# Kernel optimization log

Hardware: AMD Instinct MI355X
Metric: run time of the kernel (lower is better)

## Reference

```python
import jax, jax.numpy as jnp
import numpy as np

NUM_FEATURES = 129  # lstm_hidden + 1
GAMMA = 1.0


def _lstm(x, W_ih, W_hh, b_ih, b_hh):
    # x: [B,S,F]; W_ih: [4H,F]; W_hh: [4H,H]; gates in torch order i,f,g,o
    B, S, _ = x.shape
    H = W_hh.shape[1]
    xg = jnp.einsum('bsf,gf->bsg', x, W_ih) + b_ih  # [B,S,4H]

    def step(carry, xt):
        h, c = carry
        g = xt + h @ W_hh.T + b_hh
        i, f, gg, o = jnp.split(g, 4, axis=-1)
        c = jax.nn.sigmoid(f) * c + jax.nn.sigmoid(i) * jnp.tanh(gg)
        h = jax.nn.sigmoid(o) * jnp.tanh(c)
        return (h, c), h

    h0 = jnp.zeros((B, H), x.dtype)
    (_, _), hs = jax.lax.scan(step, (h0, h0), jnp.swapaxes(xg, 0, 1))
    return jnp.swapaxes(hs, 0, 1)  # [B,S,H]


def setup_inputs() -> dict:
    key = jax.random.key(0)
    ks = jax.random.split(key, 10)
    B, S, F, H = 16, 2048, 129, 128
    s = 0.05  # keep activations in a sane range
    return {
        'x': jax.random.normal(ks[0], (B, S, F), jnp.float32),
        'prototypes': jax.random.normal(ks[1], (B, S, F), jnp.float32),
        'W_ih': jax.random.normal(ks[2], (4 * H, F), jnp.float32) * s,
        'W_hh': jax.random.normal(ks[3], (4 * H, H), jnp.float32) * s,
        'b_ih': jax.random.normal(ks[4], (4 * H,), jnp.float32) * s,
        'b_hh': jax.random.normal(ks[5], (4 * H,), jnp.float32) * s,
        'Wc': jax.random.normal(ks[6], (4, F, F), jnp.float32) * s,
        'bc': jax.random.normal(ks[7], (4, F), jnp.float32) * s,
        'Wh': jax.random.normal(ks[8], (2, F), jnp.float32) * s,
        'bh': jax.random.normal(ks[9], (2,), jnp.float32) * s,
    }


def reference(x, prototypes, W_ih, W_hh, b_ih, b_hh, Wc, bc, Wh, bh):
    lstm_out = _lstm(x, W_ih, W_hh, b_ih, b_hh)  # [B,S,H]
    # attention path is detached in the original (numpy round-trip)
    q = jax.lax.stop_gradient(lstm_out)
    # note: scale uses num_features (embed_dim of the attention object), not H
    scores = jnp.einsum('bqh,bkh->bqk', q, q) / jnp.sqrt(jnp.float32(NUM_FEATURES))
    attn = jax.nn.softmax(scores, axis=-1)
    context = jnp.einsum('bqk,bkh->bqh', attn, q)  # [B,S,H]
    # vectorized RBF kernel vs prototypes (original does a Python loop per (i,j))
    diff = x - prototypes
    kernel_features = jnp.exp(-GAMMA * jnp.sum(diff * diff, axis=-1, keepdims=True))  # [B,S,1]
    h = jnp.concatenate([context, kernel_features], axis=-1)  # [B,S,NUM_FEATURES]
    for l in range(4):
        h = jax.nn.relu(h @ Wc[l].T + bc[l])
    logits = h @ Wh.T + bh  # [B,S,2]
    return jax.nn.log_softmax(logits, axis=-1)
```

## Files before the change

kernel.cpp:

```cpp
#include <hip/hip_runtime.h>
#include <stdint.h>

#define B_ 16
#define S_ 2048
#define F_ 129
#define H_ 128
#define G_ 512

typedef float f32x4 __attribute__((ext_vector_type(4)));
typedef float f32x4a4 __attribute__((ext_vector_type(4), aligned(4)));
typedef short s16x8 __attribute__((ext_vector_type(8)));
typedef _Float16 f16x8 __attribute__((ext_vector_type(8)));
typedef _Float16 f16x4 __attribute__((ext_vector_type(4)));

#define BAR_LDS() __asm__ volatile("s_waitcnt lgkmcnt(0)\n\ts_barrier" ::: "memory")

#define L2E 1.44269504088896f

__device__ inline unsigned short h2bits(_Float16 h) {
  union { _Float16 h; unsigned short u; } v; v.h = h; return v.u;
}
__device__ inline unsigned short f2h(float f) { return h2bits((_Float16)f); }
__device__ inline float rcp_(float x) { return __builtin_amdgcn_rcpf(x); }
__device__ inline float exp2_(float x) {
  float r; __asm__("v_exp_f32 %0, %1" : "=v"(r) : "v"(x)); return r;
}

__global__ __launch_bounds__(512, 2) void front_kernel(
    const float* __restrict__ x, const float* __restrict__ prot,
    const float* __restrict__ W_ih, const float* __restrict__ W_hh,
    const float* __restrict__ b_ih, const float* __restrict__ b_hh,
    _Float16* __restrict__ xg, unsigned short* __restrict__ qbf,
    float* __restrict__ kf, int* __restrict__ prog) {
  __shared__ __align__(16) char smem[82048];
  int tid = threadIdx.x;
  int blk = blockIdx.x;

  if (blk < 4) {
    _Float16 (*hbuf)[4 * 144] = (_Float16 (*)[4 * 144])smem;
    int w = tid >> 6, lane = tid & 63;
    int n16 = lane & 15;
    int q8 = lane >> 4;
    int ab = n16 >> 2;
    int u = (w << 4) | n16;
    int bb = blk * 4;
    f16x8 Wf[4][4];
    #pragma unroll
    for (int ty = 0; ty < 4; ++ty) {
      float gs = (ty == 2) ? (2.f * L2E) : (-L2E);
      #pragma unroll
      for (int kb = 0; kb < 4; ++kb) {
        const float* src = &W_hh[(ty * 128 + u) * H_ + kb * 32 + q8 * 8];
        f16x8 v;
        #pragma unroll
        for (int j = 0; j < 8; ++j) v[j] = (_Float16)(src[j] * gs);
        Wf[ty][kb] = v;
      }
    }
    for (int i = tid; i < 2 * 4 * 144; i += 512)
      ((_Float16*)hbuf)[i] = (_Float16)0.f;
    float c = 0.f;
    int hoff = ab * 144 + q8 * 8;
    const _Float16* h0 = &hbuf[0][hoff];
    const _Float16* h1 = &hbuf[1][hoff];
    _Float16* hw = &hbuf[0][q8 * 144 + u];
    const int hstride = 4 * 144;
    const _Float16* xb = xg + (long)(bb + q8) * S_ * G_ + u * 4;
    unsigned short* qp = qbf + (long)(bb + q8) * S_ * H_ + u - H_;
    const _Float16* xpf = xb + 4 * G_;
    while (__hip_atomic_load(&prog[0], __ATOMIC_ACQUIRE, __HIP_MEMORY_SCOPE_AGENT) < 16)
      __builtin_amdgcn_s_sleep(2);
    while (__hip_atomic_load(&prog[1], __ATOMIC_ACQUIRE, __HIP_MEMORY_SCOPE_AGENT) < 16)
      __builtin_amdgcn_s_sleep(2);
    f16x4 cur[4];
    #pragma unroll
    for (int p = 0; p < 4; ++p) cur[p] = *(const f16x4*)(xb + (long)p * G_);
    unsigned short hvp = 0;
    __syncthreads();
    for (int t = 0; t < S_; t += 4) {
      if ((t & 63) == 0 && t != 0 && t < 1984) {
        int cn = (t >> 6) + 1;
        while (__hip_atomic_load(&prog[cn], __ATOMIC_ACQUIRE, __HIP_MEMORY_SCOPE_AGENT) < 16)
          __builtin_amdgcn_s_sleep(2);
      }
      #pragma unroll
      for (int p = 0; p < 4; ++p) {
        BAR_LDS();
        const _Float16* hsrc = (p & 1) ? h0 : h1;
        f16x8 A[4];
        #pragma unroll
        for (int kb = 0; kb < 4; ++kb)
          A[kb] = *(const f16x8*)(hsrc + kb * 32);
        if (t + p > 0)
          *qp = hvp;
        qp += H_;
        f16x4 xcur = cur[p];
        cur[p] = *(const f16x4*)xpf;
        xpf += G_;
        f32x4 r0a[4], r1a[4];
        #pragma unroll
        for (int ty = 0; ty < 4; ++ty) {
          f32x4 a0, a1;
          a0[0] = (float)xcur[ty]; a0[1] = 0.f; a0[2] = 0.f; a0[3] = 0.f;
          a1[0] = 0.f; a1[1] = 0.f; a1[2] = 0.f; a1[3] = 0.f;
          a0 = __builtin_amdgcn_mfma_f32_16x16x32_f16(A[0], Wf[ty][0], a0, 0, 0, 0);
          a1 = __builtin_amdgcn_mfma_f32_16x16x32_f16(A[2], Wf[ty][2], a1, 0, 0, 0);
          a0 = __builtin_amdgcn_mfma_f32_16x16x32_f16(A[1], Wf[ty][1], a0, 0, 0, 0);
          a1 = __builtin_amdgcn_mfma_f32_16x16x32_f16(A[3], Wf[ty][3], a1, 0, 0, 0);
          r0a[ty] = a0; r1a[ty] = a1;
        }
        float g0 = r0a[0][0] + r1a[0][0];
        float g1 = r0a[1][0] + r1a[1][0];
        float g2 = r0a[2][0] + r1a[2][0];
        float g3 = r0a[3][0] + r1a[3][0];
        float ai = rcp_(1.f + exp2_(g0));
        float af = rcp_(1.f + exp2_(g1));
        float ag = 1.f - 2.f * rcp_(1.f + exp2_(g2));
        float ao = rcp_(1.f + exp2_(g3));
        c = af * c + ai * ag;
        float th = 1.f - 2.f * rcp_(1.f + exp2_(c * (2.f * L2E)));
        float hv = ao * th;
        _Float16 hf = (_Float16)hv;
        hw[(p & 1) * hstride] = hf;
        hvp = h2bits(hf);
      }
    }
    *qp = hvp;

  } else if (blk < 516) {
    _Float16 (*xs)[136] = (_Float16 (*)[136])smem;
    _Float16 (*ws)[136] = (_Float16 (*)[136])(smem + 17408);
    float* bsum = (float*)(smem + 17408 + 34816);
    int xblk = blk - 4;
    int batch = xblk & 15, chunk = xblk >> 4;
    long R0 = (long)batch * S_ + chunk * 64;
    int lane = tid & 63, w = tid >> 6;
    int tw = w & 3, hi = w >> 2;
    int l15 = lane & 15, q = lane >> 4;
    for (int it = 0; it < 4; ++it) {
      int i = tid + it * 512;
      int r = i >> 5, cx = (i & 31) * 4;
      f32x4a4 v = *(const f32x4a4*)&x[(R0 + r) * 129 + cx];
      f16x4 hq;
      #pragma unroll
      for (int j = 0; j < 4; ++j) hq[j] = (_Float16)v[j];
      *(f16x4*)&xs[r][cx] = hq;
    }
    if (tid < 64) xs[tid][128] = (_Float16)x[(R0 + tid) * 129 + 128];
    bsum[tid] = b_ih[tid] + b_hh[tid];
    __syncthreads();
    f16x8 Bf[4];
    #pragma unroll
    for (int kb = 0; kb < 4; ++kb)
      Bf[kb] = *(const f16x8*)&xs[16 * tw + l15][kb * 32 + q * 8];
    float x128 = (float)xs[16 * tw + l15][128];
    f16x4 res[16];
    #pragma unroll
    for (int cg = 0; cg < 4; ++cg) {
      __syncthreads();
      for (int it = 0; it < 8; ++it) {
        int i = tid + it * 512;
        int r = i >> 5, cc = (i & 31) * 4;
        f32x4a4 v = *(const f32x4a4*)&W_ih[(long)(cg * 128 + r) * 129 + cc];
        f16x4 hq;
        #pragma unroll
        for (int j = 0; j < 4; ++j) hq[j] = (_Float16)v[j];
        *(f16x4*)&ws[r][cc] = hq;
      }
      if (tid < 128) ws[tid][128] = (_Float16)W_ih[(long)(cg * 128 + tid) * 129 + 128];
      __syncthreads();
      float gs = (cg == 2) ? (2.f * L2E) : (-L2E);
      #pragma unroll
      for (int t = 0; t < 4; ++t) {
        int tt = hi * 4 + t;
        f32x4 acc;
        acc[0] = 0.f; acc[1] = 0.f; acc[2] = 0.f; acc[3] = 0.f;
        #pragma unroll
        for (int kb = 0; kb < 4; ++kb) {
          f16x8 Af = *(const f16x8*)&ws[tt * 16 + l15][kb * 32 + q * 8];
          acc = __builtin_amdgcn_mfma_f32_16x16x32_f16(Af, Bf[kb], acc, 0, 0, 0);
        }
        #pragma unroll
        for (int r = 0; r < 4; ++r) {
          int unit = tt * 16 + q * 4 + r;
          float vv = (acc[r] + bsum[cg * 128 + unit] + x128 * (float)ws[unit][128]) * gs;
          res[t * 4 + r][cg] = (_Float16)vv;
        }
      }
    }
    long rowbase = (R0 + 16 * tw + l15) * G_;
    #pragma unroll
    for (int t = 0; t < 4; ++t)
      #pragma unroll
      for (int r = 0; r < 4; ++r)
        *(f16x4*)&xg[rowbase + ((hi * 4 + t) * 16 + q * 4 + r) * 4] = res[t * 4 + r];
    __syncthreads();
    if (tid == 0) {
      __threadfence();
      __hip_atomic_fetch_add(&prog[chunk], 1, __ATOMIC_RELEASE, __HIP_MEMORY_SCOPE_AGENT);
    }

  } else {
    int rblk = blk - 516;
    int wave = tid >> 6, lane = tid & 63;
    for (int it = 0; it < 8; ++it) {
      long row = (long)rblk * 64 + it * 8 + wave;
      const float* xr = x + row * F_;
      const float* pr = prot + row * F_;
      float ss = 0.f;
      for (int k = lane; k < F_; k += 64) { float d = xr[k] - pr[k]; ss += d * d; }
      #pragma unroll
      for (int off = 32; off; off >>= 1) ss += __shfl_xor(ss, off, 64);
      if (lane == 0) kf[row] = __expf(-ss);
    }
  }
}

__global__ __launch_bounds__(256) void back_kernel(
    const unsigned short* __restrict__ qbf, const float* __restrict__ kf,
    const float* __restrict__ Wc, const float* __restrict__ bc,
    const float* __restrict__ Wh, const float* __restrict__ bh,
    float* __restrict__ out) {
  __shared__ __align__(16) char smem[74560];
  _Float16 (*hb)[64][136] = (_Float16 (*)[64][136])smem;
  unsigned short* Ps = (unsigned short*)(smem + 17408);
  unsigned short* Ks = (unsigned short*)(smem + 34816);
  unsigned short* VT = (unsigned short*)(smem + 34816 + 17408);
  _Float16 (*wl)[136] = (_Float16 (*)[136])(smem + 34816);
  float* bl = (float*)(smem + 34816 + 39168);

  int tid = threadIdx.x;
  int lane = tid & 63, w = tid >> 6;
  int b = blockIdx.x >> 5;
  int q0 = (blockIdx.x & 31) * 64;
  long R0 = (long)blockIdx.x * 64;
  const unsigned short* qb = qbf + (long)b * S_ * H_;
  int l15 = lane & 15;
  int q = lane >> 4;
  int koff = q * 8;

  f16x8 qfrag[4];
  #pragma unroll
  for (int kb = 0; kb < 4; ++kb)
    qfrag[kb] = *(const f16x8*)(qb + (long)(q0 + w * 16 + l15) * H_ + kb * 32 + koff);
  f32x4 oacc[8];
  #pragma unroll
  for (int n = 0; n < 8; ++n)
    #pragma unroll
    for (int r = 0; r < 4; ++r) oacc[n][r] = 0.f;
  float mrow[4], lrow[4];
  #pragma unroll
  for (int r = 0; r < 4; ++r) { mrow[r] = -1e30f; lrow[r] = 0.f; }
  const float scale = 0.08804509063256238f;
  unsigned short* Pw = Ps + w * 16 * 72;
  for (int t = 0; t < S_ / 64; ++t) {
    {
      int rr = tid >> 4;
      int c0 = (tid & 15) * 8;
      #pragma unroll
      for (int pch = 0; pch < 4; ++pch) {
        int r = pch * 16 + rr;
        s16x8 v = *(const s16x8*)(qb + (long)(t * 64 + r) * H_ + c0);
        *(s16x8*)(&Ks[r * 136 + c0]) = v;
        int rbase = r >> 3, rl = r & 7;
        #pragma unroll
        for (int i = 0; i < 8; ++i) {
          int d = c0 + i;
          VT[d * 72 + ((rbase ^ ((d >> 3) & 7)) << 3) + rl] = (unsigned short)v[i];
        }
      }
    }
    __syncthreads();
    f32x4 sacc[4];
    #pragma unroll
    for (int n = 0; n < 4; ++n) {
      f32x4 acc;
      #pragma unroll
      for (int r = 0; r < 4; ++r) acc[r] = 0.f;
      #pragma unroll
      for (int kb = 0; kb < 4; ++kb) {
        f16x8 bfrag = *(const f16x8*)(&Ks[(n * 16 + l15) * 136 + kb * 32 + koff]);
        acc = __builtin_amdgcn_mfma_f32_16x16x32_f16(qfrag[kb], bfrag, acc, 0, 0, 0);
      }
      sacc[n] = acc;
    }
    #pragma unroll
    for (int r = 0; r < 4; ++r) {
      float mx = fmaxf(fmaxf(sacc[0][r], sacc[1][r]), fmaxf(sacc[2][r], sacc[3][r]));
      #pragma unroll
      for (int m = 1; m < 16; m <<= 1) mx = fmaxf(mx, __shfl_xor(mx, m, 64));
      mx *= scale;
      float mnew = fmaxf(mrow[r], mx);
      float alpha = __expf(mrow[r] - mnew);
      mrow[r] = mnew;
      float psum = 0.f;
      #pragma unroll
      for (int n = 0; n < 4; ++n) {
        float pv = __expf(sacc[n][r] * scale - mnew);
        sacc[n][r] = pv;
        psum += pv;
      }
      #pragma unroll
      for (int m = 1; m < 16; m <<= 1) psum += __shfl_xor(psum, m, 64);
      lrow[r] = lrow[r] * alpha + psum;
      #pragma unroll
      for (int n = 0; n < 8; ++n) oacc[n][r] *= alpha;
    }
    #pragma unroll
    for (int n = 0; n < 4; ++n)
      #pragma unroll
      for (int r = 0; r < 4; ++r)
        Pw[(q * 4 + r) * 72 + n * 16 + l15] = f2h(sacc[n][r]);
    __syncthreads();
    #pragma unroll
    for (int kb = 0; kb < 2; ++kb) {
      f16x8 afrag = *(const f16x8*)(&Pw[l15 * 72 + kb * 32 + koff]);
      #pragma unroll
      for (int n = 0; n < 8; ++n) {
        int d = n * 16 + l15;
        int rb = ((kb * 32 + koff) >> 3) ^ ((d >> 3) & 7);
        f16x8 bfrag = *(const f16x8*)(&VT[d * 72 + (rb << 3)]);
        oacc[n] = __builtin_amdgcn_mfma_f32_16x16x32_f16(afrag, bfrag, oacc[n], 0, 0, 0);
      }
    }
    __syncthreads();
  }
  float rl4[4];
  #pragma unroll
  for (int r = 0; r < 4; ++r) rl4[r] = rcp_(lrow[r]);
  #pragma unroll
  for (int n = 0; n < 8; ++n)
    #pragma unroll
    for (int r = 0; r < 4; ++r)
      hb[0][w * 16 + q * 4 + r][n * 16 + l15] = (_Float16)(oacc[n][r] * rl4[r]);
  if (tid < 64) hb[0][tid][128] = (_Float16)kf[R0 + tid];

  int cur = 0;
  for (int l = 0; l < 4; ++l) {
    __syncthreads();
    for (int it = 0; it < 18; ++it) {
      int i = tid + it * 256;
      int r = i >> 5, cc = (i & 31) * 4;
      int rs = (r < 129) ? r : 128;
      f32x4a4 v = *(const f32x4a4*)&Wc[((long)l * 129 + rs) * 129 + cc];
      f16x4 hq;
      #pragma unroll
      for (int j = 0; j < 4; ++j) hq[j] = (_Float16)v[j];
      *(f16x4*)&wl[r][cc] = hq;
    }
    if (tid < 144) {
      int rs = (tid < 129) ? tid : 128;
      wl[tid][128] = (_Float16)Wc[((long)l * 129 + rs) * 129 + 128];
      bl[tid] = bc[l * 129 + rs];
    }
    __syncthreads();
    f16x8 Bf[4];
    #pragma unroll
    for (int kb = 0; kb < 4; ++kb)
      Bf[kb] = *(const f16x8*)&hb[cur][16 * w + l15][kb * 32 + q * 8];
    float h128 = (float)hb[cur][16 * w + l15][128];
    int nxt = cur ^ 1;
    #pragma unroll
    for (int t = 0; t < 9; ++t) {
      f32x4 acc;
      acc[0] = 0.f; acc[1] = 0.f; acc[2] = 0.f; acc[3] = 0.f;
      #pragma unroll
      for (int kb = 0; kb < 4; ++kb) {
        f16x8 Af = *(const f16x8*)&wl[t * 16 + l15][kb * 32 + q * 8];
        acc = __builtin_amdgcn_mfma_f32_16x16x32_f16(Af, Bf[kb], acc, 0, 0, 0);
      }
      f16x4 hv;
      #pragma unroll
      for (int r = 0; r < 4; ++r) {
        int u = t * 16 + q * 4 + r;
        float v = acc[r] + bl[u] + h128 * (float)wl[u][128];
        hv[r] = (_Float16)fmaxf(v, 0.f);
      }
      if (t < 8)
        *(f16x4*)&hb[nxt][16 * w + l15][t * 16 + q * 4] = hv;
      else if (q == 0)
        hb[nxt][16 * w + l15][128] = hv[0];
    }
    cur ^= 1;
  }
  __syncthreads();
  if (tid < 128) {
    int row = tid >> 1, j = tid & 1;
    float z = bh[j];
    const float* whp = Wh + j * 129;
    for (int k = 0; k < 129; ++k) z += (float)hb[cur][row][k] * whp[k];
    float zo = __shfl_xor(z, 1, 64);
    float mx = fmaxf(z, zo);
    float lse = mx + __logf(__expf(z - mx) + __expf(zo - mx));
    out[(R0 + row) * 2 + j] = z - lse;
  }
}

extern "C" void kernel_launch(void* const* d_in, const int* in_sizes, int n_in,
                              void* d_out, int out_size, void* d_ws, size_t ws_size,
                              hipStream_t stream) {
  const float* x    = (const float*)d_in[0];
  const float* prot = (const float*)d_in[1];
  const float* W_ih = (const float*)d_in[2];
  const float* W_hh = (const float*)d_in[3];
  const float* b_ih = (const float*)d_in[4];
  const float* b_hh = (const float*)d_in[5];
  const float* Wc   = (const float*)d_in[6];
  const float* bc   = (const float*)d_in[7];
  const float* Wh   = (const float*)d_in[8];
  const float* bh   = (const float*)d_in[9];
  float* out = (float*)d_out;
  char* ws = (char*)d_ws;
  _Float16* xgh       = (_Float16*)(ws);
  unsigned short* qbf = (unsigned short*)(ws + 33554432);
  float* kf           = (float*)(ws + 41943040);
  int* prog           = (int*)(ws + 42074112);

  hipMemsetAsync(prog, 0, 128, stream);
  hipLaunchKernelGGL(front_kernel, dim3(1028), dim3(512), 0, stream,
                     x, prot, W_ih, W_hh, b_ih, b_hh, xgh, qbf, kf, prog);
  hipLaunchKernelGGL(back_kernel, dim3(512), dim3(256), 0, stream,
                     qbf, kf, Wc, bc, Wh, bh, out);
}
```

Baseline: 1.131 ms.

## Write transposed LSTM output from recurrence and load V tile directly; single-thread flag polling

The recurrent blocks now also write each hidden value into a transposed [B,H,S] buffer, so the attention kernel can load the V^T tile with vectorized 16-byte reads instead of scattering eight scalar LDS stores per element. Spin-waiting on progress flags now happens on one thread with a longer sleep and a deadline, followed by a block barrier, rather than every thread polling. The cost is an extra strided scalar global store per step in the serial LSTM loop, plus more barriers in that loop. The deadline escape could also let the loop continue before its producers finish if they are slow.

```diff
diff --git a/kernel.cpp b/kernel.cpp
--- a/kernel.cpp
+++ b/kernel.cpp
@@ -26,15 +26,30 @@
   float r; __asm__("v_exp_f32 %0, %1" : "=v"(r) : "v"(x)); return r;
 }
 
+__device__ inline void wait_flag(int* f, int tgt, int tid, long deadline) {
+  if (tid == 0) {
+    if (__hip_atomic_load(f, __ATOMIC_RELAXED, __HIP_MEMORY_SCOPE_AGENT) < tgt) {
+      while (__hip_atomic_load(f, __ATOMIC_RELAXED, __HIP_MEMORY_SCOPE_AGENT) < tgt) {
+        __builtin_amdgcn_s_sleep(32);
+        if ((long)__builtin_amdgcn_s_memrealtime() > deadline) break;
+      }
+    }
+    (void)__hip_atomic_load(f, __ATOMIC_ACQUIRE, __HIP_MEMORY_SCOPE_AGENT);
+  }
+  __syncthreads();
+}
+
 __global__ __launch_bounds__(512, 2) void front_kernel(
     const float* __restrict__ x, const float* __restrict__ prot,
     const float* __restrict__ W_ih, const float* __restrict__ W_hh,
     const float* __restrict__ b_ih, const float* __restrict__ b_hh,
     _Float16* __restrict__ xg, unsigned short* __restrict__ qbf,
-    float* __restrict__ kf, int* __restrict__ prog) {
+    unsigned short* __restrict__ qbfT, float* __restrict__ kf,
+    int* __restrict__ prog) {
   __shared__ __align__(16) char smem[82048];
   int tid = threadIdx.x;
   int blk = blockIdx.x;
+  long deadline = (long)__builtin_amdgcn_s_memrealtime() + 4000000L;
 
   if (blk < 4) {
     _Float16 (*hbuf)[4 * 144] = (_Float16 (*)[4 * 144])smem;
@@ -67,22 +82,18 @@
     const int hstride = 4 * 144;
     const _Float16* xb = xg + (long)(bb + q8) * S_ * G_ + u * 4;
     unsigned short* qp = qbf + (long)(bb + q8) * S_ * H_ + u - H_;
+    unsigned short* qpT = qbfT + ((long)(bb + q8) * H_ + u) * S_ - 1;
     const _Float16* xpf = xb + 4 * G_;
-    while (__hip_atomic_load(&prog[0], __ATOMIC_ACQUIRE, __HIP_MEMORY_SCOPE_AGENT) < 16)
-      __builtin_amdgcn_s_sleep(2);
-    while (__hip_atomic_load(&prog[1], __ATOMIC_ACQUIRE, __HIP_MEMORY_SCOPE_AGENT) < 16)
-      __builtin_amdgcn_s_sleep(2);
+    wait_flag(&prog[0], 16, tid, deadline);
+    wait_flag(&prog[1], 16, tid, deadline);
     f16x4 cur[4];
     #pragma unroll
     for (int p = 0; p < 4; ++p) cur[p] = *(const f16x4*)(xb + (long)p * G_);
     unsigned short hvp = 0;
     __syncthreads();
     for (int t = 0; t < S_; t += 4) {
-      if ((t & 63) == 0 && t != 0 && t < 1984) {
-        int cn = (t >> 6) + 1;
-        while (__hip_atomic_load(&prog[cn], __ATOMIC_ACQUIRE, __HIP_MEMORY_SCOPE_AGENT) < 16)
-          __builtin_amdgcn_s_sleep(2);
-      }
+      if ((t & 63) == 0 && t != 0 && t < 1984)
+        wait_flag(&prog[(t >> 6) + 1], 16, tid, deadline);
       #pragma unroll
       for (int p = 0; p < 4; ++p) {
         BAR_LDS();
@@ -91,9 +102,12 @@
         #pragma unroll
         for (int kb = 0; kb < 4; ++kb)
           A[kb] = *(const f16x8*)(hsrc + kb * 32);
-        if (t + p > 0)
+        if (t + p > 0) {
           *qp = hvp;
+          *qpT = hvp;
+        }
         qp += H_;
+        qpT += 1;
         f16x4 xcur = cur[p];
         cur[p] = *(const f16x4*)xpf;
         xpf += G_;
@@ -126,6 +140,7 @@
       }
     }
     *qp = hvp;
+    *qpT = hvp;
 
   } else if (blk < 516) {
     _Float16 (*xs)[136] = (_Float16 (*)[136])smem;
@@ -217,7 +232,8 @@
 }
 
 __global__ __launch_bounds__(256) void back_kernel(
-    const unsigned short* __restrict__ qbf, const float* __restrict__ kf,
+    const unsigned short* __restrict__ qbf, const unsigned short* __restrict__ qbfT,
+    const float* __restrict__ kf,
     const float* __restrict__ Wc, const float* __restrict__ bc,
     const float* __restrict__ Wh, const float* __restrict__ bh,
     float* __restrict__ out) {
@@ -235,6 +251,7 @@
   int q0 = (blockIdx.x & 31) * 64;
   long R0 = (long)blockIdx.x * 64;
   const unsigned short* qb = qbf + (long)b * S_ * H_;
+  const unsigned short* qbT = qbfT + (long)b * H_ * S_;
   int l15 = lane & 15;
   int q = lane >> 4;
   int koff = q * 8;
@@ -260,14 +277,15 @@
       #pragma unroll
       for (int pch = 0; pch < 4; ++pch) {
         int r = pch * 16 + rr;
-        s16x8 v = *(const s16x8*)(qb + (long)(t * 64 + r) * H_ + c0);
-        *(s16x8*)(&Ks[r * 136 + c0]) = v;
-        int rbase = r >> 3, rl = r & 7;
-        #pragma unroll
-        for (int i = 0; i < 8; ++i) {
-          int d = c0 + i;
-          VT[d * 72 + ((rbase ^ ((d >> 3) & 7)) << 3) + rl] = (unsigned short)v[i];
-        }
+        *(s16x8*)(&Ks[r * 136 + c0]) =
+            *(const s16x8*)(qb + (long)(t * 64 + r) * H_ + c0);
+      }
+      #pragma unroll
+      for (int vt = 0; vt < 4; ++vt) {
+        int idx = tid + vt * 256;
+        int d = idx >> 3, tg = idx & 7;
+        s16x8 v = *(const s16x8*)(qbT + (long)d * S_ + t * 64 + tg * 8);
+        *(s16x8*)(&VT[d * 72 + ((tg ^ ((d >> 3) & 7)) << 3)]) = v;
       }
     }
     __syncthreads();
@@ -411,14 +429,15 @@
   const float* bh   = (const float*)d_in[9];
   float* out = (float*)d_out;
   char* ws = (char*)d_ws;
-  _Float16* xgh       = (_Float16*)(ws);
-  unsigned short* qbf = (unsigned short*)(ws + 33554432);
-  float* kf           = (float*)(ws + 41943040);
-  int* prog           = (int*)(ws + 42074112);
+  _Float16* xgh        = (_Float16*)(ws);
+  unsigned short* qbf  = (unsigned short*)(ws + 33554432);
+  unsigned short* qbfT = (unsigned short*)(ws + 41943040);
+  float* kf            = (float*)(ws + 50331648);
+  int* prog            = (int*)(ws + 50462720);
 
   hipMemsetAsync(prog, 0, 128, stream);
   hipLaunchKernelGGL(front_kernel, dim3(1028), dim3(512), 0, stream,
-                     x, prot, W_ih, W_hh, b_ih, b_hh, xgh, qbf, kf, prog);
+                     x, prot, W_ih, W_hh, b_ih, b_hh, xgh, qbf, qbfT, kf, prog);
   hipLaunchKernelGGL(back_kernel, dim3(512), dim3(256), 0, stream,
-                     qbf, kf, Wc, bc, Wh, bh, out);
-}
+                     qbf, qbfT, kf, Wc, bc, Wh, bh, out);
+}
```

New measurement: 1.334 ms. 1.18x slower.

## Prefetch next K/V tile into registers, raise MFMA priority, single-thread flag waits

Applied to the files above, without the earlier changes.

The attention loop now loads the next 64-row K/V tile from global memory into registers while the current tile is written into LDS, so global load latency overlaps with compute. MFMA sections are wrapped in s_setprio to favour matrix work across waves. The LSTM blocks' spin-waits on producer progress flags are changed so one thread polls with a longer sleep and a timeout, then the block synchronises, which cuts polling traffic from every thread. The timeout could let the LSTM read data before it is ready if producers are slow, and the prefetch adds register pressure.

```diff
diff --git a/kernel.cpp b/kernel.cpp
--- a/kernel.cpp
+++ b/kernel.cpp
@@ -24,6 +24,19 @@
 __device__ inline float rcp_(float x) { return __builtin_amdgcn_rcpf(x); }
 __device__ inline float exp2_(float x) {
   float r; __asm__("v_exp_f32 %0, %1" : "=v"(r) : "v"(x)); return r;
+}
+
+__device__ inline void wait_flag(int* f, int tgt, int tid, long deadline) {
+  if (tid == 0) {
+    if (__hip_atomic_load(f, __ATOMIC_RELAXED, __HIP_MEMORY_SCOPE_AGENT) < tgt) {
+      while (__hip_atomic_load(f, __ATOMIC_RELAXED, __HIP_MEMORY_SCOPE_AGENT) < tgt) {
+        __builtin_amdgcn_s_sleep(32);
+        if ((long)__builtin_amdgcn_s_memrealtime() > deadline) break;
+      }
+    }
+    (void)__hip_atomic_load(f, __ATOMIC_ACQUIRE, __HIP_MEMORY_SCOPE_AGENT);
+  }
+  __syncthreads();
 }
 
 __global__ __launch_bounds__(512, 2) void front_kernel(
@@ -35,6 +48,7 @@
   __shared__ __align__(16) char smem[82048];
   int tid = threadIdx.x;
   int blk = blockIdx.x;
+  long deadline = (long)__builtin_amdgcn_s_memrealtime() + 4000000L;
 
   if (blk < 4) {
     _Float16 (*hbuf)[4 * 144] = (_Float16 (*)[4 * 144])smem;
@@ -68,21 +82,16 @@
     const _Float16* xb = xg + (long)(bb + q8) * S_ * G_ + u * 4;
     unsigned short* qp = qbf + (long)(bb + q8) * S_ * H_ + u - H_;
     const _Float16* xpf = xb + 4 * G_;
-    while (__hip_atomic_load(&prog[0], __ATOMIC_ACQUIRE, __HIP_MEMORY_SCOPE_AGENT) < 16)
-      __builtin_amdgcn_s_sleep(2);
-    while (__hip_atomic_load(&prog[1], __ATOMIC_ACQUIRE, __HIP_MEMORY_SCOPE_AGENT) < 16)
-      __builtin_amdgcn_s_sleep(2);
+    wait_flag(&prog[0], 16, tid, deadline);
+    wait_flag(&prog[1], 16, tid, deadline);
     f16x4 cur[4];
     #pragma unroll
     for (int p = 0; p < 4; ++p) cur[p] = *(const f16x4*)(xb + (long)p * G_);
     unsigned short hvp = 0;
     __syncthreads();
     for (int t = 0; t < S_; t += 4) {
-      if ((t & 63) == 0 && t != 0 && t < 1984) {
-        int cn = (t >> 6) + 1;
-        while (__hip_atomic_load(&prog[cn], __ATOMIC_ACQUIRE, __HIP_MEMORY_SCOPE_AGENT) < 16)
-          __builtin_amdgcn_s_sleep(2);
-      }
+      if ((t & 63) == 0 && t != 0 && t < 1984)
+        wait_flag(&prog[(t >> 6) + 1], 16, tid, deadline);
       #pragma unroll
       for (int p = 0; p < 4; ++p) {
         BAR_LDS();
@@ -253,14 +262,18 @@
   for (int r = 0; r < 4; ++r) { mrow[r] = -1e30f; lrow[r] = 0.f; }
   const float scale = 0.08804509063256238f;
   unsigned short* Pw = Ps + w * 16 * 72;
+  int rr = tid >> 4;
+  int c0 = (tid & 15) * 8;
+  s16x8 vstage[4];
+  #pragma unroll
+  for (int pch = 0; pch < 4; ++pch)
+    vstage[pch] = *(const s16x8*)(qb + (long)(pch * 16 + rr) * H_ + c0);
   for (int t = 0; t < S_ / 64; ++t) {
     {
-      int rr = tid >> 4;
-      int c0 = (tid & 15) * 8;
       #pragma unroll
       for (int pch = 0; pch < 4; ++pch) {
         int r = pch * 16 + rr;
-        s16x8 v = *(const s16x8*)(qb + (long)(t * 64 + r) * H_ + c0);
+        s16x8 v = vstage[pch];
         *(s16x8*)(&Ks[r * 136 + c0]) = v;
         int rbase = r >> 3, rl = r & 7;
         #pragma unroll
@@ -269,9 +282,15 @@
           VT[d * 72 + ((rbase ^ ((d >> 3) & 7)) << 3) + rl] = (unsigned short)v[i];
         }
       }
+      if (t + 1 < S_ / 64) {
+        #pragma unroll
+        for (int pch = 0; pch < 4; ++pch)
+          vstage[pch] = *(const s16x8*)(qb + (long)((t + 1) * 64 + pch * 16 + rr) * H_ + c0);
+      }
     }
     __syncthreads();
     f32x4 sacc[4];
+    __builtin_amdgcn_s_setprio(1);
     #pragma unroll
     for (int n = 0; n < 4; ++n) {
       f32x4 acc;
@@ -284,6 +303,7 @@
       }
       sacc[n] = acc;
     }
+    __builtin_amdgcn_s_setprio(0);
     #pragma unroll
     for (int r = 0; r < 4; ++r) {
       float mx = fmaxf(fmaxf(sacc[0][r], sacc[1][r]), fmaxf(sacc[2][r], sacc[3][r]));
@@ -312,6 +332,7 @@
       for (int r = 0; r < 4; ++r)
         Pw[(q * 4 + r) * 72 + n * 16 + l15] = f2h(sacc[n][r]);
     __syncthreads();
+    __builtin_amdgcn_s_setprio(1);
     #pragma unroll
     for (int kb = 0; kb < 2; ++kb) {
       f16x8 afrag = *(const f16x8*)(&Pw[l15 * 72 + kb * 32 + koff]);
@@ -323,6 +344,7 @@
         oacc[n] = __builtin_amdgcn_mfma_f32_16x16x32_f16(afrag, bfrag, oacc[n], 0, 0, 0);
       }
     }
+    __builtin_amdgcn_s_setprio(0);
     __syncthreads();
   }
   float rl4[4];
```

After: 1.121 ms. No clear change (-0.9%).
